# Kernel optimization log

Hardware: AMD Instinct MI355X
Metric: run time of the kernel (lower is better)

The kernel has to match this reference:

```python
import jax, jax.numpy as jnp
import numpy as np

N = 100000
E = 1600000

def _gc(x, W, b, src, tgt, w):
    # GraphConvolution: transform, gather per-edge messages from src,
    # weight by the sparse aggregation matrix entries (Mtgt values),
    # scatter-sum into target nodes, add bias.
    support = x @ W                       # [N, out]
    msg = support[src] * w[:, None]        # [E, out]
    agg = jax.ops.segment_sum(msg, tgt, num_segments=N)  # [N, out]
    return agg + b

def setup_inputs() -> dict:
    key = jax.random.key(0)
    ks = jax.random.split(key, 10)
    d_in, d_h, d_out = 128, 64, 40
    x = jax.random.normal(ks[0], (N, d_in), dtype=jnp.float32)
    src = jax.random.randint(ks[1], (E,), 0, N)
    tgt = jax.random.randint(ks[2], (E,), 0, N)
    mtgt_w = jax.random.uniform(ks[3], (E,), dtype=jnp.float32)
    def glorot(k, shape):
        lim = 1.0 / np.sqrt(shape[0])
        return jax.random.uniform(k, shape, jnp.float32, -lim, lim)
    return {
        'x': x, 'src': src, 'tgt': tgt, 'mtgt_w': mtgt_w,
        'W0': glorot(ks[4], (d_in, d_h)), 'b0': jnp.zeros((d_h,), jnp.float32),
        'W1': glorot(ks[5], (d_h, d_h)),  'b1': jnp.zeros((d_h,), jnp.float32),
        'W2': glorot(ks[6], (d_h, d_h)),  'b2': jnp.zeros((d_h,), jnp.float32),
        'W3': glorot(ks[7], (d_h, d_out)),'b3': jnp.zeros((d_out,), jnp.float32),
    }

def reference(x, src, tgt, mtgt_w, W0, b0, W1, b1, W2, b2, W3, b3):
    # RESK forward, eval mode (dropout = identity), nlayers=4, residue_layers=1.
    h = jax.nn.relu(_gc(x, W0, b0, src, tgt, mtgt_w))
    # middle layer 1: residual block (r = h; h = relu(gc(h)) + r)
    r = h
    h = jax.nn.relu(_gc(h, W1, b1, src, tgt, mtgt_w)) + r
    # middle layer 2: residual block
    r = h
    h = jax.nn.relu(_gc(h, W2, b2, src, tgt, mtgt_w)) + r
    out = _gc(h, W3, b3, src, tgt, mtgt_w)
    return jax.nn.log_softmax(out, axis=1)
```

## Files before the change

kernel.cpp:

```cpp
#include <hip/hip_runtime.h>
#include <cstdint>
#include <cstddef>
#include <math.h>


typedef unsigned int uint;
typedef unsigned short ushort;
typedef unsigned char uchar;

typedef __attribute__((ext_vector_type(8))) short bf16x8;
typedef __attribute__((ext_vector_type(4))) float f32x4;
typedef __attribute__((ext_vector_type(2))) float f32x2;

constexpr int NB_ROWS = 256;
constexpr int CHUNK   = 2048;
constexpr int CAP     = 4608;

__device__ __forceinline__ uint f2bf(float f) {
    uint u = __float_as_uint(f);
    return (u + 0x7FFFu + ((u >> 16) & 1u)) >> 16;
}

__global__ void zero_ints(int* __restrict__ p, int n) {
    int i = blockIdx.x * blockDim.x + threadIdx.x;
    if (i < n) p[i] = 0;
}

__global__ void prep_wt(const float* __restrict__ W0, const float* __restrict__ W1,
                        const float* __restrict__ W2, const float* __restrict__ W3,
                        ushort* __restrict__ wt0, ushort* __restrict__ wt1,
                        ushort* __restrict__ wt2, ushort* __restrict__ wt3) {
    int i = blockIdx.x * 256 + threadIdx.x;
    if (i < 64 * 128) {
        int c = i >> 7, k = i & 127;
        wt0[i] = (ushort)f2bf(W0[k * 64 + c]);
    }
    if (i < 64 * 64) {
        int c = i >> 6, k = i & 63;
        wt1[i] = (ushort)f2bf(W1[k * 64 + c]);
        wt2[i] = (ushort)f2bf(W2[k * 64 + c]);
        wt3[i] = (c < 40) ? (ushort)f2bf(W3[k * 40 + c]) : (ushort)0;
    }
}

__global__ __launch_bounds__(512) void bucket_kernel(const int* __restrict__ src,
                                                     const int* __restrict__ tgt,
                                                     const float* __restrict__ w,
                                                     int* __restrict__ bcur,
                                                     uint* __restrict__ bkt,
                                                     uchar* __restrict__ brow,
                                                     int E, int NB) {
    __shared__ uint binned[CHUNK];
    __shared__ ushort binb[CHUNK];
    __shared__ uchar binr[CHUNK];
    __shared__ int hist[512];
    __shared__ int sc[512];
    __shared__ int cur[512];
    __shared__ int gbase[512];
    int tid = threadIdx.x;
    int e0 = blockIdx.x * CHUNK;
    int cnt = min(CHUNK, E - e0);
    hist[tid] = 0;
    __syncthreads();
    for (int i = tid; i < cnt; i += 512) atomicAdd(&hist[tgt[e0 + i] >> 8], 1);
    __syncthreads();
    int v = hist[tid];
    sc[tid] = v;
    __syncthreads();
    for (int off = 1; off < 512; off <<= 1) {
        int t = (tid >= off) ? sc[tid - off] : 0;
        __syncthreads();
        sc[tid] += t;
        __syncthreads();
    }
    int excl = sc[tid] - v;
    if (tid < NB && v > 0) gbase[tid] = atomicAdd(&bcur[tid], v);
    __syncthreads();
    hist[tid] = excl;
    cur[tid] = excl;
    __syncthreads();
    for (int i = tid; i < cnt; i += 512) {
        int t = tgt[e0 + i];
        int b = t >> 8;
        int r = atomicAdd(&cur[b], 1);
        float wf = w[e0 + i];
        uint w15 = (uint)(int)(wf * 32767.f + 0.5f);
        if (w15 > 32767u) w15 = 32767u;
        binned[r] = (uint)src[e0 + i] | (w15 << 17);
        binb[r] = (ushort)b;
        binr[r] = (uchar)(t & 255);
    }
    __syncthreads();
    for (int i = tid; i < cnt; i += 512) {
        int b = binb[i];
        int dst = gbase[b] + (i - hist[b]);
        if (dst < CAP) {
            bkt[(size_t)b * CAP + dst] = binned[i];
            brow[(size_t)b * CAP + dst] = binr[i];
        }
    }
}

__global__ void bscan_kernel(const int* __restrict__ bcur, int* __restrict__ bbase,
                             int* __restrict__ row_start, int NB, int N) {
    __shared__ int sd[512];
    int tid = threadIdx.x;
    int tot = (tid < NB) ? min(bcur[tid], CAP) : 0;
    sd[tid] = tot;
    __syncthreads();
    for (int off = 1; off < 512; off <<= 1) {
        int t = (tid >= off) ? sd[tid - off] : 0;
        __syncthreads();
        sd[tid] += t;
        __syncthreads();
    }
    if (tid < NB) bbase[tid] = sd[tid] - tot;
    if (tid == 511) row_start[N] = sd[511];
}

__global__ __launch_bounds__(1024) void rowsort_kernel(const uint* __restrict__ bkt,
                                                       const uchar* __restrict__ brow,
                                                       const int* __restrict__ bcur,
                                                       const int* __restrict__ bbase,
                                                       uint* __restrict__ csr,
                                                       int* __restrict__ row_start, int N) {
    __shared__ int hist[256];
    __shared__ int offs[256];
    int b = blockIdx.x;
    int tid = threadIdx.x;
    int cnt = min(bcur[b], CAP);
    const uint* win = bkt + (size_t)b * CAP;
    const uchar* wrow = brow + (size_t)b * CAP;
    if (tid < 256) hist[tid] = 0;
    __syncthreads();
    uint en[5];
    uchar er[5];
    int ne = 0;
#pragma unroll
    for (int k = 0; k < 5; ++k) {
        int i = tid + k * 1024;
        if (i < cnt) {
            en[k] = win[i];
            er[k] = wrow[i];
            atomicAdd(&hist[er[k]], 1);
            ne = k + 1;
        }
    }
    __syncthreads();
    int v = 0;
    if (tid < 256) { v = hist[tid]; offs[tid] = v; }
    __syncthreads();
    for (int off = 1; off < 256; off <<= 1) {
        int t = 0;
        if (tid < 256 && tid >= off) t = offs[tid - off];
        __syncthreads();
        if (tid < 256) offs[tid] += t;
        __syncthreads();
    }
    int gb = bbase[b];
    if (tid < 256) {
        int excl = offs[tid] - v;
        int row = (b << 8) + tid;
        if (row < N) row_start[row] = gb + excl;
        hist[tid] = excl;
    }
    __syncthreads();
#pragma unroll
    for (int k = 0; k < 5; ++k) {
        if (k < ne) {
            int pos = atomicAdd(&hist[er[k]], 1);
            csr[gb + pos] = en[k];
        }
    }
}

template <int K>
__global__ __launch_bounds__(256) void gemm_mfma(const float* __restrict__ H,
                                                 const ushort* __restrict__ Wt,
                                                 uint* __restrict__ out, int n) {
    constexpr int NT = K / 32;
    __shared__ ushort alds[64 * K];
    int tid = threadIdx.x;
    int nbase = blockIdx.x * 64;
    int rows = min(64, n - nbase);

    const float4* Hg = (const float4*)(H + (size_t)nbase * K);
#pragma unroll
    for (int it = 0; it < K / 16; ++it) {
        int i = tid + it * 256;
        int r = i / (K / 4);
        int c4 = i % (K / 4);
        if (r < rows) {
            float4 v = Hg[i];
            uint2 pk;
            pk.x = f2bf(v.x) | (f2bf(v.y) << 16);
            pk.y = f2bf(v.z) | (f2bf(v.w) << 16);
            uint bcol = ((uint)(c4 * 8)) ^ (((uint)(r & 7)) << 4);
            *(uint2*)((char*)alds + r * (K * 2) + bcol) = pk;
        }
    }

    int wv = __builtin_amdgcn_readfirstlane(tid >> 6);
    int l = tid & 63;
    int lr = l & 15;
    int lh = l >> 4;

    bf16x8 wf[4][NT];
#pragma unroll
    for (int ct = 0; ct < 4; ++ct)
#pragma unroll
        for (int ks = 0; ks < NT; ++ks)
            wf[ct][ks] = *(const bf16x8*)(const void*)(Wt + (ct * 16 + lr) * K + ks * 32 + lh * 8);

    __syncthreads();

    f32x4 acc[4];
#pragma unroll
    for (int ct = 0; ct < 4; ++ct) acc[ct] = (f32x4){0.f, 0.f, 0.f, 0.f};

    int row = wv * 16 + lr;
#pragma unroll
    for (int ks = 0; ks < NT; ++ks) {
        uint bcol = ((uint)(ks * 64 + lh * 16)) ^ (((uint)(row & 7)) << 4);
        bf16x8 hf = *(const bf16x8*)((const char*)alds + row * (K * 2) + bcol);
#pragma unroll
        for (int ct = 0; ct < 4; ++ct)
            acc[ct] = __builtin_amdgcn_mfma_f32_16x16x32_bf16(wf[ct][ks], hf, acc[ct], 0, 0, 0);
    }

    int node = nbase + row;
    if (node < n) {
        uint* orow = out + (size_t)node * 16;
#pragma unroll
        for (int ct = 0; ct < 4; ++ct) {
            uint p = 0;
            p = __builtin_amdgcn_cvt_pk_fp8_f32(acc[ct][0], acc[ct][1], p, false);
            p = __builtin_amdgcn_cvt_pk_fp8_f32(acc[ct][2], acc[ct][3], p, true);
            orow[ct * 4 + lh] = p;
        }
    }
}

__device__ __forceinline__ float wval(uint d) {
    return (float)(d >> 17) * (1.0f / 32767.f);
}

__device__ __forceinline__ void agg4_body(const uchar* __restrict__ sb,
                                          const int* __restrict__ row_start,
                                          const uint* __restrict__ csr, int n0,
                                          int lane, int N, float& a0, float& a1,
                                          float& a2, float& a3) {
    int g = lane >> 4;
    uint voff = (uint)((lane & 15) << 2);

    int idx = n0 + lane;
    if (idx > N) idx = N;
    int rsv = (lane <= 4) ? row_start[idx] : 0;
    int rs0 = __shfl(rsv, 0);
    int myb = __shfl(rsv, g);
    int mye = __shfl(rsv, g + 1);
    int tend = __shfl(rsv, 4);

    for (int W0 = rs0; W0 < tend; W0 += 64) {
        int ei = W0 + lane;
        uint entry = (ei < tend) ? csr[ei] : 0u;
        int lo = myb - W0;
        if (lo < 0) lo = 0;
        int hi = mye - W0;
        if (hi > 64) hi = 64;
        int cnt = hi - lo;
        if (cnt < 0) cnt = 0;
        int mx = cnt;
        mx = max(mx, __shfl_xor(mx, 16));
        mx = max(mx, __shfl_xor(mx, 32));
        for (int o = 0; o < mx; o += 4) {
            uint dd[4];
            uint uu[4];
#pragma unroll
            for (int j = 0; j < 4; ++j) {
                int p = (lo + o + j) & 63;
                uint d = (uint)__builtin_amdgcn_ds_bpermute(p << 2, (int)entry);
                dd[j] = ((o + j) < cnt) ? d : 0u;
            }
#pragma unroll
            for (int j = 0; j < 4; ++j)
                uu[j] = *(const uint*)(sb + (((dd[j] & 0x1FFFFu) << 6) | voff));
#pragma unroll
            for (int j = 0; j < 4; ++j) {
                float wv = wval(dd[j]);
                f32x2 flo = __builtin_amdgcn_cvt_pk_f32_fp8(uu[j], false);
                f32x2 fhi = __builtin_amdgcn_cvt_pk_f32_fp8(uu[j], true);
                a0 = fmaf(flo[0], wv, a0);
                a1 = fmaf(flo[1], wv, a1);
                a2 = fmaf(fhi[0], wv, a2);
                a3 = fmaf(fhi[1], wv, a3);
            }
        }
    }
}

__global__ __launch_bounds__(256) void agg64_kernel(const uchar* __restrict__ sb,
                                                    const int* __restrict__ row_start,
                                                    const uint* __restrict__ csr,
                                                    const float* __restrict__ bias,
                                                    const float* __restrict__ resid,
                                                    float* __restrict__ out, int n) {
    int wid = (blockIdx.x * blockDim.x + threadIdx.x) >> 6;
    int lane = threadIdx.x & 63;
    int n0 = wid * 4;
    if (n0 >= n) return;
    float a0 = 0.f, a1 = 0.f, a2 = 0.f, a3 = 0.f;
    agg4_body(sb, row_start, csr, n0, lane, n, a0, a1, a2, a3);
    int g = lane >> 4;
    int c = lane & 15;
    int nd = n0 + g;
    if (nd < n) {
        float4 bv = *(const float4*)(bias + 4 * c);
        float h0 = fmaxf(a0 + bv.x, 0.f);
        float h1 = fmaxf(a1 + bv.y, 0.f);
        float h2 = fmaxf(a2 + bv.z, 0.f);
        float h3 = fmaxf(a3 + bv.w, 0.f);
        if (resid) {
            float4 rv = *(const float4*)(resid + (size_t)nd * 64 + 4 * c);
            h0 += rv.x;
            h1 += rv.y;
            h2 += rv.z;
            h3 += rv.w;
        }
        *(float4*)(out + (size_t)nd * 64 + 4 * c) = make_float4(h0, h1, h2, h3);
    }
}

__global__ __launch_bounds__(256) void agg_final_kernel(const uchar* __restrict__ sb,
                                                        const int* __restrict__ row_start,
                                                        const uint* __restrict__ csr,
                                                        const float* __restrict__ bias,
                                                        float* __restrict__ out, int n) {
    int wid = (blockIdx.x * blockDim.x + threadIdx.x) >> 6;
    int lane = threadIdx.x & 63;
    int n0 = wid * 4;
    if (n0 >= n) return;
    float a0 = 0.f, a1 = 0.f, a2 = 0.f, a3 = 0.f;
    agg4_body(sb, row_start, csr, n0, lane, n, a0, a1, a2, a3);
    int g = lane >> 4;
    int c = lane & 15;
    int nd = n0 + g;
    bool act = c < 10;
    float v0 = -INFINITY, v1 = -INFINITY, v2 = -INFINITY, v3 = -INFINITY;
    if (act) {
        float4 bv = *(const float4*)(bias + 4 * c);
        v0 = a0 + bv.x;
        v1 = a1 + bv.y;
        v2 = a2 + bv.z;
        v3 = a3 + bv.w;
    }
    float m = fmaxf(fmaxf(v0, v1), fmaxf(v2, v3));
#pragma unroll
    for (int d = 1; d < 16; d <<= 1) m = fmaxf(m, __shfl_xor(m, d));
    float ex = act ? (expf(v0 - m) + expf(v1 - m) + expf(v2 - m) + expf(v3 - m)) : 0.f;
#pragma unroll
    for (int d = 1; d < 16; d <<= 1) ex += __shfl_xor(ex, d);
    float lse = m + logf(ex);
    if (act && nd < n)
        *(float4*)(out + (size_t)nd * 40 + 4 * c) =
            make_float4(v0 - lse, v1 - lse, v2 - lse, v3 - lse);
}

extern "C" void kernel_launch(void* const* d_in, const int* in_sizes, int n_in,
                              void* d_out, int out_size, void* d_ws, size_t ws_size,
                              hipStream_t stream) {
    const float* x   = (const float*)d_in[0];
    const int*   src = (const int*)d_in[1];
    const int*   tgt = (const int*)d_in[2];
    const float* mw  = (const float*)d_in[3];
    const float* W0  = (const float*)d_in[4];
    const float* b0  = (const float*)d_in[5];
    const float* W1  = (const float*)d_in[6];
    const float* b1  = (const float*)d_in[7];
    const float* W2  = (const float*)d_in[8];
    const float* b2  = (const float*)d_in[9];
    const float* W3  = (const float*)d_in[10];
    const float* b3  = (const float*)d_in[11];
    float* out = (float*)d_out;

    const int N = in_sizes[0] / 128;
    const int E = in_sizes[1];
    const int NB = (N + NB_ROWS - 1) / NB_ROWS;

    char* p = (char*)d_ws;
    auto carve = [&](size_t bytes) {
        char* r = p;
        p += (bytes + 255) & ~size_t(255);
        return r;
    };
    int*    bcur      = (int*)carve((size_t)NB * 4);
    int*    bbase     = (int*)carve((size_t)NB * 4);
    int*    row_start = (int*)carve((size_t)(N + 1) * 4);
    uint*   bkt       = (uint*)carve((size_t)NB * CAP * 4);
    uchar*  brow      = (uchar*)carve((size_t)NB * CAP);
    uint*   csr       = (uint*)carve((size_t)E * 4);
    uchar*  support   = (uchar*)carve((size_t)N * 64);
    float*  h         = (float*)carve((size_t)N * 64 * 4);
    ushort* wt0       = (ushort*)carve((size_t)64 * 128 * 2);
    ushort* wt1       = (ushort*)carve((size_t)64 * 64 * 2);
    ushort* wt2       = (ushort*)carve((size_t)64 * 64 * 2);
    ushort* wt3       = (ushort*)carve((size_t)64 * 64 * 2);

    int gblocks = (N + 63) / 64;
    int ablocks = (N + 15) / 16;

    zero_ints<<<(NB + 255) / 256, 256, 0, stream>>>(bcur, NB);
    prep_wt<<<32, 256, 0, stream>>>(W0, W1, W2, W3, wt0, wt1, wt2, wt3);
    bucket_kernel<<<(E + CHUNK - 1) / CHUNK, 512, 0, stream>>>(src, tgt, mw, bcur, bkt, brow, E, NB);
    bscan_kernel<<<1, 512, 0, stream>>>(bcur, bbase, row_start, NB, N);
    rowsort_kernel<<<NB, 1024, 0, stream>>>(bkt, brow, bcur, bbase, csr, row_start, N);

    gemm_mfma<128><<<gblocks, 256, 0, stream>>>(x, wt0, (uint*)support, N);
    agg64_kernel<<<ablocks, 256, 0, stream>>>(support, row_start, csr, b0, nullptr, h, N);
    gemm_mfma<64><<<gblocks, 256, 0, stream>>>(h, wt1, (uint*)support, N);
    agg64_kernel<<<ablocks, 256, 0, stream>>>(support, row_start, csr, b1, h, h, N);
    gemm_mfma<64><<<gblocks, 256, 0, stream>>>(h, wt2, (uint*)support, N);
    agg64_kernel<<<ablocks, 256, 0, stream>>>(support, row_start, csr, b2, h, h, N);
    gemm_mfma<64><<<gblocks, 256, 0, stream>>>(h, wt3, (uint*)support, N);
    agg_final_kernel<<<ablocks, 256, 0, stream>>>(support, row_start, csr, b3, out, N);
}
```

Baseline: 334.5 us.

## Aggregate eight nodes per wavefront with 8-byte gathers and prefetched CSR

The aggregation kernels now assign eight target nodes per wavefront, using 8 lanes per node that each gather 8 FP8 features (uint2) instead of 16 lanes with 4. The next 64-entry CSR window is loaded before the current one is processed. This halves the number of wavefronts, widens each gather, and overlaps CSR load latency with work. The cost is more accumulator registers and a wider max-count reduction across 8 groups, which may add idle iterations when degrees differ within a wavefront.

```diff
diff --git a/kernel.cpp b/kernel.cpp
--- a/kernel.cpp
+++ b/kernel.cpp
@@ -245,25 +245,26 @@
     return (float)(d >> 17) * (1.0f / 32767.f);
 }
 
-__device__ __forceinline__ void agg4_body(const uchar* __restrict__ sb,
+__device__ __forceinline__ void agg8_body(const uchar* __restrict__ sb,
                                           const int* __restrict__ row_start,
                                           const uint* __restrict__ csr, int n0,
-                                          int lane, int N, float& a0, float& a1,
-                                          float& a2, float& a3) {
-    int g = lane >> 4;
-    uint voff = (uint)((lane & 15) << 2);
+                                          int lane, int N, float* a) {
+    int g = lane >> 3;
+    uint voff = (uint)((lane & 7) << 3);
 
     int idx = n0 + lane;
     if (idx > N) idx = N;
-    int rsv = (lane <= 4) ? row_start[idx] : 0;
+    int rsv = (lane <= 8) ? row_start[idx] : 0;
     int rs0 = __shfl(rsv, 0);
     int myb = __shfl(rsv, g);
     int mye = __shfl(rsv, g + 1);
-    int tend = __shfl(rsv, 4);
-
-    for (int W0 = rs0; W0 < tend; W0 += 64) {
-        int ei = W0 + lane;
-        uint entry = (ei < tend) ? csr[ei] : 0u;
+    int tend = __shfl(rsv, 8);
+
+    int W0 = rs0;
+    uint cur = (W0 + lane < tend) ? csr[W0 + lane] : 0u;
+    for (; W0 < tend; W0 += 64) {
+        int ein = W0 + 64 + lane;
+        uint nxt = (ein < tend) ? csr[ein] : 0u;
         int lo = myb - W0;
         if (lo < 0) lo = 0;
         int hi = mye - W0;
@@ -271,31 +272,39 @@
         int cnt = hi - lo;
         if (cnt < 0) cnt = 0;
         int mx = cnt;
+        mx = max(mx, __shfl_xor(mx, 8));
         mx = max(mx, __shfl_xor(mx, 16));
         mx = max(mx, __shfl_xor(mx, 32));
         for (int o = 0; o < mx; o += 4) {
             uint dd[4];
-            uint uu[4];
+            uint2 uu[4];
 #pragma unroll
             for (int j = 0; j < 4; ++j) {
                 int p = (lo + o + j) & 63;
-                uint d = (uint)__builtin_amdgcn_ds_bpermute(p << 2, (int)entry);
+                uint d = (uint)__builtin_amdgcn_ds_bpermute(p << 2, (int)cur);
                 dd[j] = ((o + j) < cnt) ? d : 0u;
             }
 #pragma unroll
             for (int j = 0; j < 4; ++j)
-                uu[j] = *(const uint*)(sb + (((dd[j] & 0x1FFFFu) << 6) | voff));
+                uu[j] = *(const uint2*)(sb + (((dd[j] & 0x1FFFFu) << 6) | voff));
 #pragma unroll
             for (int j = 0; j < 4; ++j) {
                 float wv = wval(dd[j]);
-                f32x2 flo = __builtin_amdgcn_cvt_pk_f32_fp8(uu[j], false);
-                f32x2 fhi = __builtin_amdgcn_cvt_pk_f32_fp8(uu[j], true);
-                a0 = fmaf(flo[0], wv, a0);
-                a1 = fmaf(flo[1], wv, a1);
-                a2 = fmaf(fhi[0], wv, a2);
-                a3 = fmaf(fhi[1], wv, a3);
+                f32x2 f0 = __builtin_amdgcn_cvt_pk_f32_fp8(uu[j].x, false);
+                f32x2 f1 = __builtin_amdgcn_cvt_pk_f32_fp8(uu[j].x, true);
+                f32x2 f2 = __builtin_amdgcn_cvt_pk_f32_fp8(uu[j].y, false);
+                f32x2 f3 = __builtin_amdgcn_cvt_pk_f32_fp8(uu[j].y, true);
+                a[0] = fmaf(f0[0], wv, a[0]);
+                a[1] = fmaf(f0[1], wv, a[1]);
+                a[2] = fmaf(f1[0], wv, a[2]);
+                a[3] = fmaf(f1[1], wv, a[3]);
+                a[4] = fmaf(f2[0], wv, a[4]);
+                a[5] = fmaf(f2[1], wv, a[5]);
+                a[6] = fmaf(f3[0], wv, a[6]);
+                a[7] = fmaf(f3[1], wv, a[7]);
             }
         }
+        cur = nxt;
     }
 }
 
@@ -307,27 +316,34 @@
                                                     float* __restrict__ out, int n) {
     int wid = (blockIdx.x * blockDim.x + threadIdx.x) >> 6;
     int lane = threadIdx.x & 63;
-    int n0 = wid * 4;
+    int n0 = wid * 8;
     if (n0 >= n) return;
-    float a0 = 0.f, a1 = 0.f, a2 = 0.f, a3 = 0.f;
-    agg4_body(sb, row_start, csr, n0, lane, n, a0, a1, a2, a3);
-    int g = lane >> 4;
-    int c = lane & 15;
+    float a[8];
+#pragma unroll
+    for (int i = 0; i < 8; ++i) a[i] = 0.f;
+    agg8_body(sb, row_start, csr, n0, lane, n, a);
+    int g = lane >> 3;
+    int c = lane & 7;
     int nd = n0 + g;
     if (nd < n) {
-        float4 bv = *(const float4*)(bias + 4 * c);
-        float h0 = fmaxf(a0 + bv.x, 0.f);
-        float h1 = fmaxf(a1 + bv.y, 0.f);
-        float h2 = fmaxf(a2 + bv.z, 0.f);
-        float h3 = fmaxf(a3 + bv.w, 0.f);
+        float4 b0 = *(const float4*)(bias + 8 * c);
+        float4 b1 = *(const float4*)(bias + 8 * c + 4);
+        float h0 = fmaxf(a[0] + b0.x, 0.f);
+        float h1 = fmaxf(a[1] + b0.y, 0.f);
+        float h2 = fmaxf(a[2] + b0.z, 0.f);
+        float h3 = fmaxf(a[3] + b0.w, 0.f);
+        float h4 = fmaxf(a[4] + b1.x, 0.f);
+        float h5 = fmaxf(a[5] + b1.y, 0.f);
+        float h6 = fmaxf(a[6] + b1.z, 0.f);
+        float h7 = fmaxf(a[7] + b1.w, 0.f);
         if (resid) {
-            float4 rv = *(const float4*)(resid + (size_t)nd * 64 + 4 * c);
-            h0 += rv.x;
-            h1 += rv.y;
-            h2 += rv.z;
-            h3 += rv.w;
-        }
-        *(float4*)(out + (size_t)nd * 64 + 4 * c) = make_float4(h0, h1, h2, h3);
+            float4 r0 = *(const float4*)(resid + (size_t)nd * 64 + 8 * c);
+            float4 r1 = *(const float4*)(resid + (size_t)nd * 64 + 8 * c + 4);
+            h0 += r0.x; h1 += r0.y; h2 += r0.z; h3 += r0.w;
+            h4 += r1.x; h5 += r1.y; h6 += r1.z; h7 += r1.w;
+        }
+        *(float4*)(out + (size_t)nd * 64 + 8 * c) = make_float4(h0, h1, h2, h3);
+        *(float4*)(out + (size_t)nd * 64 + 8 * c + 4) = make_float4(h4, h5, h6, h7);
     }
 }
 
@@ -338,32 +354,45 @@
                                                         float* __restrict__ out, int n) {
     int wid = (blockIdx.x * blockDim.x + threadIdx.x) >> 6;
     int lane = threadIdx.x & 63;
-    int n0 = wid * 4;
+    int n0 = wid * 8;
     if (n0 >= n) return;
-    float a0 = 0.f, a1 = 0.f, a2 = 0.f, a3 = 0.f;
-    agg4_body(sb, row_start, csr, n0, lane, n, a0, a1, a2, a3);
-    int g = lane >> 4;
-    int c = lane & 15;
+    float a[8];
+#pragma unroll
+    for (int i = 0; i < 8; ++i) a[i] = 0.f;
+    agg8_body(sb, row_start, csr, n0, lane, n, a);
+    int g = lane >> 3;
+    int c = lane & 7;
     int nd = n0 + g;
-    bool act = c < 10;
-    float v0 = -INFINITY, v1 = -INFINITY, v2 = -INFINITY, v3 = -INFINITY;
+    bool act = c < 5;
+    float v[8];
+#pragma unroll
+    for (int i = 0; i < 8; ++i) v[i] = -INFINITY;
     if (act) {
-        float4 bv = *(const float4*)(bias + 4 * c);
-        v0 = a0 + bv.x;
-        v1 = a1 + bv.y;
-        v2 = a2 + bv.z;
-        v3 = a3 + bv.w;
-    }
-    float m = fmaxf(fmaxf(v0, v1), fmaxf(v2, v3));
-#pragma unroll
-    for (int d = 1; d < 16; d <<= 1) m = fmaxf(m, __shfl_xor(m, d));
-    float ex = act ? (expf(v0 - m) + expf(v1 - m) + expf(v2 - m) + expf(v3 - m)) : 0.f;
-#pragma unroll
-    for (int d = 1; d < 16; d <<= 1) ex += __shfl_xor(ex, d);
+        float4 b0 = *(const float4*)(bias + 8 * c);
+        float4 b1 = *(const float4*)(bias + 8 * c + 4);
+        v[0] = a[0] + b0.x; v[1] = a[1] + b0.y;
+        v[2] = a[2] + b0.z; v[3] = a[3] + b0.w;
+        v[4] = a[4] + b1.x; v[5] = a[5] + b1.y;
+        v[6] = a[6] + b1.z; v[7] = a[7] + b1.w;
+    }
+    float m = v[0];
+#pragma unroll
+    for (int i = 1; i < 8; ++i) m = fmaxf(m, v[i]);
+#pragma unroll
+    for (int d = 1; d < 8; d <<= 1) m = fmaxf(m, __shfl_xor(m, d));
+    float ex = 0.f;
+    if (act) {
+#pragma unroll
+        for (int i = 0; i < 8; ++i) ex += expf(v[i] - m);
+    }
+#pragma unroll
+    for (int d = 1; d < 8; d <<= 1) ex += __shfl_xor(ex, d);
     float lse = m + logf(ex);
-    if (act && nd < n)
-        *(float4*)(out + (size_t)nd * 40 + 4 * c) =
-            make_float4(v0 - lse, v1 - lse, v2 - lse, v3 - lse);
+    if (act && nd < n) {
+        float* orow = out + (size_t)nd * 40 + 8 * c;
+        *(float4*)orow = make_float4(v[0] - lse, v[1] - lse, v[2] - lse, v[3] - lse);
+        *(float4*)(orow + 4) = make_float4(v[4] - lse, v[5] - lse, v[6] - lse, v[7] - lse);
+    }
 }
 
 extern "C" void kernel_launch(void* const* d_in, const int* in_sizes, int n_in,
@@ -407,7 +436,7 @@
     ushort* wt3       = (ushort*)carve((size_t)64 * 64 * 2);
 
     int gblocks = (N + 63) / 64;
-    int ablocks = (N + 15) / 16;
+    int ablocks = (N + 31) / 32;
 
     zero_ints<<<(NB + 255) / 256, 256, 0, stream>>>(bcur, NB);
     prep_wt<<<32, 256, 0, stream>>>(W0, W1, W2, W3, wt0, wt1, wt2, wt3);
```

Measured after the change: 349.7 us. +4.5%, slower.
